# Kernel optimization log

Measured on AMD Instinct MI355X. Metric: run time of the kernel, lower is better.

## Reference

```python
import jax, jax.numpy as jnp
import numpy as np

VOCAB = 50000
CUTOFF = [20000, 40000]
EMBED_DIM = 1024
FACTOR = 4.0
PAD = 1


def setup_inputs() -> dict:
    key = jax.random.key(0)
    k0, k1, k2, k3, k4, k5 = jax.random.split(key, 6)
    ends = [0] + CUTOFF + [VOCAB]
    dims = [int(EMBED_DIM // FACTOR ** i) for i in range(len(ends) - 1)]  # [1024, 256, 64]
    sizes = [ends[i + 1] - ends[i] for i in range(len(ends) - 1)]          # [20000, 20000, 10000]
    input_ids = jax.random.randint(k0, (8, 4096), 0, VOCAB, dtype=jnp.int32)
    # nn.Embedding default init: N(0, 1)
    emb0 = jax.random.normal(k1, (sizes[0], dims[0]), dtype=jnp.float32)
    emb1 = jax.random.normal(k2, (sizes[1], dims[1]), dtype=jnp.float32)
    emb2 = jax.random.normal(k3, (sizes[2], dims[2]), dtype=jnp.float32)
    # projection weight [embedding_dim, dim_i], init N(0, dim_i^-0.5)
    proj1 = jax.random.normal(k4, (EMBED_DIM, dims[1]), dtype=jnp.float32) * dims[1] ** -0.5
    proj2 = jax.random.normal(k5, (EMBED_DIM, dims[2]), dtype=jnp.float32) * dims[2] ** -0.5
    return {"input_ids": input_ids, "emb0": emb0, "emb1": emb1, "emb2": emb2,
            "proj1": proj1, "proj2": proj2}


def reference(input_ids, emb0, emb1, emb2, proj1, proj2):
    ends = [0] + CUTOFF + [VOCAB]
    tables = [emb0, emb1, emb2]
    projs = [None, proj1, proj2]
    result = jnp.zeros(input_ids.shape + (EMBED_DIM,), dtype=emb0.dtype)
    for i, (tab, proj) in enumerate(zip(tables, projs)):
        l, r = ends[i], ends[i + 1]
        # padding_idx zeroes the local pad row of each cluster table
        tab = tab.at[PAD].set(0.0)
        local = jnp.clip(input_ids - l, 0, r - l - 1)  # safe gather index
        e = tab[local]                                  # [B, S, dim_i]
        if proj is not None:
            e = jnp.einsum('bsd,ed->bse', e, proj)      # Linear(dim_i -> EMBED_DIM), no bias
        in_cluster = ((input_ids >= l) & (input_ids < r))[..., None]
        result = jnp.where(in_cluster, e, result)
    return result
```

## Files before the change

kernel.cpp:

```cpp
#include <hip/hip_runtime.h>


constexpr int NTOK = 8 * 4096;
constexpr int C1 = 20000;
constexpr int C2 = 40000;
constexpr int DIM = 1024;
constexpr int PAD = 1;
constexpr int K1 = 256, K2 = 64;
constexpr int NP1 = DIM * K1;
constexpr int NP2 = DIM * K2;
constexpr int GTOK = 32;
constexpr int NB1 = NTOK / GTOK;
constexpr int NSEG = 64;
constexpr int SEGW = 512;
constexpr int CROW = DIM + 4;
constexpr int SMEM_BYTES = 16 * CROW * 4;

typedef unsigned short u16;
typedef unsigned int u32;
typedef unsigned long long u64;
typedef __attribute__((ext_vector_type(8))) short bf16x8;
typedef __attribute__((ext_vector_type(4))) float f32x4;

__device__ __forceinline__ u16 f2bf(float f) {
    u32 u = __builtin_bit_cast(u32, f);
    return (u16)((u + 0x7FFFu + ((u >> 16) & 1u)) >> 16);
}

template<int K>
__device__ __forceinline__ void cvt_body(int idx, const float* __restrict__ src,
                                         u16* __restrict__ dst) {
    constexpr int KS = K / 32;
    int lane = idx & 63;
    int rest = idx >> 6;
    int kstep = rest % KS;
    int ntile = rest / KS;
    int n = ntile * 16 + (lane & 15);
    int k = kstep * 32 + (lane >> 4) * 8;
    const float4* p = (const float4*)(src + (size_t)n * K + k);
    float4 a = p[0], b = p[1];
    u16 t[8] = {f2bf(a.x), f2bf(a.y), f2bf(a.z), f2bf(a.w),
                f2bf(b.x), f2bf(b.y), f2bf(b.z), f2bf(b.w)};
    *(int4*)(dst + (size_t)idx * 8) = *(const int4*)t;
}

__global__ __launch_bounds__(512) void prep_k(const int* __restrict__ ids,
        u16* __restrict__ list1, u16* __restrict__ list2,
        int* __restrict__ cnt1, int* __restrict__ cnt2,
        const float* __restrict__ proj1, const float* __restrict__ proj2,
        u16* __restrict__ projL1, u16* __restrict__ projL2) {
    int b = blockIdx.x;
    int tid = threadIdx.x;
    if (b >= 64) {
        if (b < 128) cvt_body<K1>((b - 64) * 512 + tid, proj1, projL1);
        else         cvt_body<K2>((b - 128) * 512 + tid, proj2, projL2);
        return;
    }
    __shared__ int woff1[8], woff2[8];
    int i = b * SEGW + tid;
    int id = ids[i];
    bool in1 = (id >= C1) & (id < C2);
    bool in2 = (id >= C2);
    u64 b1 = __ballot(in1);
    u64 b2 = __ballot(in2);
    int wave = tid >> 6, lane = tid & 63;
    if (lane == 0) { woff1[wave] = __popcll(b1); woff2[wave] = __popcll(b2); }
    __syncthreads();
    if (tid == 0) {
        int t1 = 0, t2 = 0;
        #pragma unroll
        for (int w = 0; w < 8; ++w) {
            int c1 = woff1[w]; woff1[w] = t1; t1 += c1;
            int c2 = woff2[w]; woff2[w] = t2; t2 += c2;
        }
        cnt1[b] = t1;
        cnt2[b] = t2;
    }
    __syncthreads();
    u64 lt = (lane == 63) ? ~0ull >> 1 : (1ull << lane) - 1;
    if (in1) list1[b * SEGW + woff1[wave] + __popcll(b1 & lt)] = (u16)i;
    if (in2) list2[b * SEGW + woff2[wave] + __popcll(b2 & lt)] = (u16)i;
}

template<int K>
__device__ __forceinline__ void gemm_body(int b, const int* __restrict__ ids,
        const float* __restrict__ emb, const u16* __restrict__ projL,
        const u16* __restrict__ list, const int* __restrict__ cnt,
        int base, float* __restrict__ out, char* __restrict__ sm,
        u16* __restrict__ s_tok, int* __restrict__ s_loc, int* __restrict__ s_pref) {
    constexpr int K8 = K / 8;
    constexpr int KS = K / 32;
    constexpr int LROW = K + 8;
    u16* A = (u16*)sm;
    float* Cs = (float*)sm;
    int t0 = b * GTOK;
    int tid = threadIdx.x;

    if (tid < 64) {
        int c = cnt[tid];
        #pragma unroll
        for (int d = 1; d < 64; d <<= 1) {
            int y = __shfl_up(c, d);
            if ((tid & 63) >= d) c += y;
        }
        s_pref[tid + 1] = c;
        if (tid == 0) s_pref[0] = 0;
    }
    __syncthreads();
    int count = s_pref[NSEG];
    if (t0 >= count) return;
    int nt_valid = min(GTOK, count - t0);

    if (tid < GTOK) {
        int tokidx = 0, loc = -1;
        if (tid < nt_valid) {
            int g = t0 + tid;
            int lo = 0, hi = NSEG - 1;
            #pragma unroll
            for (int it = 0; it < 6; ++it) {
                int mid = (lo + hi + 1) >> 1;
                if (s_pref[mid] <= g) lo = mid; else hi = mid - 1;
            }
            tokidx = list[lo * SEGW + (g - s_pref[lo])];
            loc = ids[tokidx] - base;
            if (loc == PAD) loc = -1;
        }
        s_tok[tid] = (u16)tokidx;
        s_loc[tid] = loc;
    }
    __syncthreads();

    for (int c = tid; c < GTOK * K8; c += 512) {
        int m = c / K8, k8 = c % K8;
        int loc = s_loc[m];
        float4 v0 = make_float4(0.f,0.f,0.f,0.f), v1 = v0;
        if (loc >= 0) {
            const float4* p = (const float4*)(emb + (size_t)loc * K) + k8 * 2;
            v0 = p[0]; v1 = p[1];
        }
        u16 t[8] = {f2bf(v0.x), f2bf(v0.y), f2bf(v0.z), f2bf(v0.w),
                    f2bf(v1.x), f2bf(v1.y), f2bf(v1.z), f2bf(v1.w)};
        *(int4*)&A[m * LROW + k8 * 8] = *(const int4*)t;
    }
    __syncthreads();

    int wave = tid >> 6;
    int lane = tid & 63;
    int lr = lane & 15;
    int lk = (lane >> 4) * 8;
    const bf16x8* Bfrag = (const bf16x8*)projL;

    f32x4 acc[2][8] = {};
    for (int ks = 0; ks < KS; ++ks) {
        bf16x8 a0 = *(const bf16x8*)&A[lr * LROW + ks * 32 + lk];
        bf16x8 a1 = *(const bf16x8*)&A[(16 + lr) * LROW + ks * 32 + lk];
        #pragma unroll
        for (int nt = 0; nt < 8; ++nt) {
            bf16x8 bb = Bfrag[((size_t)((wave * 8 + nt) * KS + ks)) * 64 + lane];
            acc[0][nt] = __builtin_amdgcn_mfma_f32_16x16x32_bf16(a0, bb, acc[0][nt], 0, 0, 0);
            acc[1][nt] = __builtin_amdgcn_mfma_f32_16x16x32_bf16(a1, bb, acc[1][nt], 0, 0, 0);
        }
    }
    __syncthreads();

    int rbase = (lane >> 4) * 4;
    #pragma unroll
    for (int mh = 0; mh < 2; ++mh) {
        #pragma unroll
        for (int nt = 0; nt < 8; ++nt) {
            #pragma unroll
            for (int r = 0; r < 4; ++r)
                Cs[(rbase + r) * CROW + wave * 128 + nt * 16 + lr] = acc[mh][nt][r];
        }
        __syncthreads();
        #pragma unroll
        for (int k = 0; k < 8; ++k) {
            int idx = k * 512 + tid;
            int row = idx >> 8;
            int col4 = idx & 255;
            int trow = mh * 16 + row;
            if (trow < nt_valid) {
                const float* s = &Cs[row * CROW + col4 * 4];
                float4 v = make_float4(s[0], s[1], s[2], s[3]);
                *(float4*)(out + (size_t)s_tok[trow] * DIM + col4 * 4) = v;
            }
        }
        __syncthreads();
    }
}

__global__ __launch_bounds__(512, 4) void fused_k(const int* __restrict__ ids,
        const float* __restrict__ emb0, const float* __restrict__ emb1,
        const float* __restrict__ emb2, const u16* __restrict__ projL1,
        const u16* __restrict__ projL2, const u16* __restrict__ list1,
        const u16* __restrict__ list2, const int* __restrict__ cnt1,
        const int* __restrict__ cnt2, float* __restrict__ out) {
    __shared__ __align__(16) char smem[SMEM_BYTES];
    __shared__ u16 s_tok[GTOK];
    __shared__ int s_loc[GTOK];
    __shared__ int s_pref[NSEG + 1];
    int b = blockIdx.x;
    int stripe = b / 6;
    int role = (b + stripe) % 6;
    if (role == 0) {
        gemm_body<K1>(stripe, ids, emb1, projL1, list1, cnt1, C1, out,
                      smem, s_tok, s_loc, s_pref);
        return;
    }
    if (role == 1) {
        gemm_body<K2>(stripe, ids, emb2, projL2, list2, cnt2, C2, out,
                      smem, s_tok, s_loc, s_pref);
        return;
    }
    int cb = stripe * 4 + (role - 2);
    int tbase = cb * 8;
    int tid = threadIdx.x;
    const float4* e4 = (const float4*)emb0;
    float4* o4 = (float4*)out;
    #pragma unroll
    for (int r = 0; r < 4; ++r) {
        int j = r * 512 + tid;
        int tok = tbase + (j >> 8);
        int d4 = j & 255;
        int id = ids[tok];
        if (id < C1) {
            float4 v = make_float4(0.f, 0.f, 0.f, 0.f);
            if (id != PAD) v = e4[(size_t)id * 256 + d4];
            o4[(size_t)tok * 256 + d4] = v;
        }
    }
}

extern "C" void kernel_launch(void* const* d_in, const int* in_sizes, int n_in,
                              void* d_out, int out_size, void* d_ws, size_t ws_size,
                              hipStream_t stream) {
    const int*   ids   = (const int*)d_in[0];
    const float* emb0  = (const float*)d_in[1];
    const float* emb1  = (const float*)d_in[2];
    const float* emb2  = (const float*)d_in[3];
    const float* proj1 = (const float*)d_in[4];
    const float* proj2 = (const float*)d_in[5];
    float* out = (float*)d_out;

    int* cnt1   = (int*)d_ws;
    int* cnt2   = cnt1 + NSEG;
    u16* list1  = (u16*)(cnt2 + NSEG);
    u16* list2  = list1 + NTOK;
    u16* projL1 = list2 + NTOK;
    u16* projL2 = projL1 + NP1;

    prep_k<<<144, 512, 0, stream>>>(ids, list1, list2, cnt1, cnt2,
                                    proj1, proj2, projL1, projL2);
    fused_k<<<NB1 * 6, 512, 0, stream>>>(ids, emb0, emb1, emb2,
                                         projL1, projL2, list1, list2,
                                         cnt1, cnt2, out);
}
```

Measured before the change: 51.87 us.

## Move emb0 gather-copy from GEMM kernel into prep kernel

The cluster-0 embedding copy blocks move out of the fused GEMM launch and into the prep kernel, which now launches 144 prep blocks plus 4096 copy blocks with a higher occupancy hint. The GEMM kernel is left with only the two projection roles. The goal is to overlap the bandwidth-heavy copy with the small prep work and let the GEMM kernel's blocks use the whole device. The cost is that the copy can no longer overlap with GEMM compute, and the prep kernel becomes much longer before the GEMMs can start.

Result: slower. 65.32 us (+25.9%).

```diff
diff --git a/kernel.cpp b/kernel.cpp
--- a/kernel.cpp
+++ b/kernel.cpp
@@ -10,9 +10,10 @@
 constexpr int NP1 = DIM * K1;
 constexpr int NP2 = DIM * K2;
 constexpr int GTOK = 32;
-constexpr int NB1 = NTOK / GTOK;
+constexpr int NGB = NTOK / GTOK;
 constexpr int NSEG = 64;
 constexpr int SEGW = 512;
+constexpr int NCPY = NTOK / 8;
 constexpr int CROW = DIM + 4;
 constexpr int SMEM_BYTES = 16 * CROW * 4;
 
@@ -44,13 +45,32 @@
     *(int4*)(dst + (size_t)idx * 8) = *(const int4*)t;
 }
 
-__global__ __launch_bounds__(512) void prep_k(const int* __restrict__ ids,
+__global__ __launch_bounds__(512, 8) void copyprep_k(const int* __restrict__ ids,
+        const float* __restrict__ emb0, float* __restrict__ out,
         u16* __restrict__ list1, u16* __restrict__ list2,
         int* __restrict__ cnt1, int* __restrict__ cnt2,
         const float* __restrict__ proj1, const float* __restrict__ proj2,
         u16* __restrict__ projL1, u16* __restrict__ projL2) {
     int b = blockIdx.x;
     int tid = threadIdx.x;
+    if (b >= 144) {
+        int tbase = (b - 144) * 8;
+        const float4* e4 = (const float4*)emb0;
+        float4* o4 = (float4*)out;
+        #pragma unroll
+        for (int r = 0; r < 4; ++r) {
+            int j = r * 512 + tid;
+            int tok = tbase + (j >> 8);
+            int d4 = j & 255;
+            int id = ids[tok];
+            if (id < C1) {
+                float4 v = make_float4(0.f, 0.f, 0.f, 0.f);
+                if (id != PAD) v = e4[(size_t)id * 256 + d4];
+                o4[(size_t)tok * 256 + d4] = v;
+            }
+        }
+        return;
+    }
     if (b >= 64) {
         if (b < 128) cvt_body<K1>((b - 64) * 512 + tid, proj1, projL1);
         else         cvt_body<K2>((b - 128) * 512 + tid, proj2, projL2);
@@ -189,46 +209,25 @@
     }
 }
 
-__global__ __launch_bounds__(512, 4) void fused_k(const int* __restrict__ ids,
-        const float* __restrict__ emb0, const float* __restrict__ emb1,
-        const float* __restrict__ emb2, const u16* __restrict__ projL1,
-        const u16* __restrict__ projL2, const u16* __restrict__ list1,
-        const u16* __restrict__ list2, const int* __restrict__ cnt1,
-        const int* __restrict__ cnt2, float* __restrict__ out) {
+__global__ __launch_bounds__(512, 4) void gemm_k(const int* __restrict__ ids,
+        const float* __restrict__ emb1, const float* __restrict__ emb2,
+        const u16* __restrict__ projL1, const u16* __restrict__ projL2,
+        const u16* __restrict__ list1, const u16* __restrict__ list2,
+        const int* __restrict__ cnt1, const int* __restrict__ cnt2,
+        float* __restrict__ out) {
     __shared__ __align__(16) char smem[SMEM_BYTES];
     __shared__ u16 s_tok[GTOK];
     __shared__ int s_loc[GTOK];
     __shared__ int s_pref[NSEG + 1];
     int b = blockIdx.x;
-    int stripe = b / 6;
-    int role = (b + stripe) % 6;
-    if (role == 0) {
+    int stripe = b >> 1;
+    int role = (b + stripe) & 1;
+    if (role == 0)
         gemm_body<K1>(stripe, ids, emb1, projL1, list1, cnt1, C1, out,
                       smem, s_tok, s_loc, s_pref);
-        return;
-    }
-    if (role == 1) {
+    else
         gemm_body<K2>(stripe, ids, emb2, projL2, list2, cnt2, C2, out,
                       smem, s_tok, s_loc, s_pref);
-        return;
-    }
-    int cb = stripe * 4 + (role - 2);
-    int tbase = cb * 8;
-    int tid = threadIdx.x;
-    const float4* e4 = (const float4*)emb0;
-    float4* o4 = (float4*)out;
-    #pragma unroll
-    for (int r = 0; r < 4; ++r) {
-        int j = r * 512 + tid;
-        int tok = tbase + (j >> 8);
-        int d4 = j & 255;
-        int id = ids[tok];
-        if (id < C1) {
-            float4 v = make_float4(0.f, 0.f, 0.f, 0.f);
-            if (id != PAD) v = e4[(size_t)id * 256 + d4];
-            o4[(size_t)tok * 256 + d4] = v;
-        }
-    }
 }
 
 extern "C" void kernel_launch(void* const* d_in, const int* in_sizes, int n_in,
@@ -249,9 +248,9 @@
     u16* projL1 = list2 + NTOK;
     u16* projL2 = projL1 + NP1;
 
-    prep_k<<<144, 512, 0, stream>>>(ids, list1, list2, cnt1, cnt2,
-                                    proj1, proj2, projL1, projL2);
-    fused_k<<<NB1 * 6, 512, 0, stream>>>(ids, emb0, emb1, emb2,
-                                         projL1, projL2, list1, list2,
-                                         cnt1, cnt2, out);
-}
+    copyprep_k<<<144 + NCPY, 512, 0, stream>>>(ids, emb0, out, list1, list2,
+                                               cnt1, cnt2, proj1, proj2,
+                                               projL1, projL2);
+    gemm_k<<<NGB * 2, 512, 0, stream>>>(ids, emb1, emb2, projL1, projL2,
+                                        list1, list2, cnt1, cnt2, out);
+}
```
